# Kernel tuning notes

Hardware: AMD Instinct MI355X
Metric: run time of the kernel (lower is better)

## Reference

```python
import jax, jax.numpy as jnp
import numpy as np
import math

D_MODEL = 1024
N_HEADS = 16
HEAD_DIM = D_MODEL // N_HEADS
FF_DIM = 4096
EPS = 1e-5


def setup_inputs() -> dict:
    key = jax.random.key(0)
    ks = jax.random.split(key, 18)
    s = 0.02
    inp = {
        "x": jax.random.normal(ks[0], (4, 2048, D_MODEL), dtype=jnp.float32),
        "wq": jax.random.normal(ks[1], (D_MODEL, D_MODEL), dtype=jnp.float32) * s,
        "bq": jnp.zeros((D_MODEL,), jnp.float32),
        "wk": jax.random.normal(ks[2], (D_MODEL, D_MODEL), dtype=jnp.float32) * s,
        "bk": jnp.zeros((D_MODEL,), jnp.float32),
        "wv": jax.random.normal(ks[3], (D_MODEL, D_MODEL), dtype=jnp.float32) * s,
        "bv": jnp.zeros((D_MODEL,), jnp.float32),
        "wo": jax.random.normal(ks[4], (D_MODEL, D_MODEL), dtype=jnp.float32) * s,
        "bo": jnp.zeros((D_MODEL,), jnp.float32),
        "w1": jax.random.normal(ks[5], (FF_DIM, D_MODEL), dtype=jnp.float32) * s,
        "b1": jnp.zeros((FF_DIM,), jnp.float32),
        "w2": jax.random.normal(ks[6], (D_MODEL, FF_DIM), dtype=jnp.float32) * s,
        "b2": jnp.zeros((D_MODEL,), jnp.float32),
        "g1": jnp.ones((D_MODEL,), jnp.float32),
        "beta1": jnp.zeros((D_MODEL,), jnp.float32),
        "g2": jnp.ones((D_MODEL,), jnp.float32),
        "beta2": jnp.zeros((D_MODEL,), jnp.float32),
    }
    return inp


def _layernorm(x, g, b):
    mu = jnp.mean(x, axis=-1, keepdims=True)
    var = jnp.mean(jnp.square(x - mu), axis=-1, keepdims=True)
    return (x - mu) * jax.lax.rsqrt(var + EPS) * g + b


def _block(x, wq, bq, wk, bk, wv, bv, wo, bo, w1, b1, w2, b2, g1, beta1, g2, beta2):
    B, S, _ = x.shape
    # projections (torch Linear: x @ W.T + b)
    q = (x @ wq.T + bq).reshape(B, S, N_HEADS, HEAD_DIM)
    k = (x @ wk.T + bk).reshape(B, S, N_HEADS, HEAD_DIM)
    v = (x @ wv.T + bv).reshape(B, S, N_HEADS, HEAD_DIM)
    scores = jnp.einsum("bqhd,bkhd->bhqk", q, k) / math.sqrt(HEAD_DIM)
    attn = jax.nn.softmax(scores, axis=-1)
    o = jnp.einsum("bhqk,bkhd->bqhd", attn, v).reshape(B, S, D_MODEL)
    attn_out = o @ wo.T + bo
    x = _layernorm(x + attn_out, g1, beta1)
    h = jax.nn.gelu(x @ w1.T + b1, approximate=False)
    ff = h @ w2.T + b2
    return _layernorm(x + ff, g2, beta2)


def reference(x, wq, bq, wk, bk, wv, bv, wo, bo, w1, b1, w2, b2, g1, beta1, g2, beta2):
    return _block(x, wq, bq, wk, bk, wv, bv, wo, bo, w1, b1, w2, b2, g1, beta1, g2, beta2)
```

## Files before the change

kernel.cpp:

```cpp
#include <hip/hip_runtime.h>
#include <hip/hip_bf16.h>
#include <math.h>


typedef __attribute__((ext_vector_type(8))) short short8;
typedef __attribute__((ext_vector_type(4))) float f32x4;

__device__ __forceinline__ unsigned short f2bf(float f) {
  unsigned int u = __builtin_bit_cast(unsigned int, f);
  u = (u + 0x7fffu + ((u >> 16) & 1u)) >> 16;
  return (unsigned short)u;
}
__device__ __forceinline__ float bf2f(unsigned short h) {
  unsigned int u = ((unsigned int)h) << 16;
  return __builtin_bit_cast(float, u);
}
__device__ __forceinline__ f32x4 mfma16(short8 a, short8 b, f32x4 c) {
  return __builtin_amdgcn_mfma_f32_16x16x32_bf16(a, b, c, 0, 0, 0);
}
__device__ __forceinline__ void gload16(const void* g, void* l) {
  __builtin_amdgcn_global_load_lds((const __attribute__((address_space(1))) void*)g,
                                   (__attribute__((address_space(3))) void*)l, 16, 0, 0);
}

__global__ void cast_f32_bf16(const float* __restrict__ in,
                              unsigned short* __restrict__ out, int n4) {
  for (int i = blockIdx.x * blockDim.x + threadIdx.x; i < n4;
       i += gridDim.x * blockDim.x) {
    float4 v = ((const float4*)in)[i];
    ushort4 o;
    o.x = f2bf(v.x); o.y = f2bf(v.y); o.z = f2bf(v.z); o.w = f2bf(v.w);
    ((ushort4*)out)[i] = o;
  }
}

template<int EPI>
__global__ void gemm_bt(const unsigned short* __restrict__ A,
                        const unsigned short* __restrict__ W,
                        const float* __restrict__ bias,
                        unsigned short* __restrict__ C,
                        int M, int N, int K) {
  __shared__ unsigned short As[128 * 64];
  __shared__ unsigned short Bs[128 * 64];
  const int t = threadIdx.x;
  const int lane = t & 63, w = t >> 6;
  const int l15 = lane & 15, l4 = lane >> 4;
  const int m0 = blockIdx.y * 128, n0 = blockIdx.x * 128;
  const int wr = (w >> 1) * 64, wc = (w & 1) * 64;
  f32x4 acc[4][4] = {};
  const int srow = t >> 3;
  const int scol = (t & 7) * 16;

  for (int k0 = 0; k0 < K; k0 += 64) {
    __syncthreads();
#pragma unroll
    for (int r = 0; r < 4; ++r) {
      int row = r * 32 + srow;
      gload16((const char*)(A + (size_t)(m0 + row) * K + k0) + scol,
              (char*)As + row * 128 + scol);
    }
#pragma unroll
    for (int r = 0; r < 4; ++r) {
      int row = r * 32 + srow;
      gload16((const char*)(W + (size_t)(n0 + row) * K + k0) + scol,
              (char*)Bs + row * 128 + scol);
    }
    __syncthreads();
#pragma unroll
    for (int ks = 0; ks < 2; ++ks) {
      short8 af[4], bfr[4];
#pragma unroll
      for (int m = 0; m < 4; ++m)
        af[m] = *(const short8*)((const char*)As + (wr + m * 16 + l15) * 128 +
                                 ks * 64 + l4 * 16);
#pragma unroll
      for (int n = 0; n < 4; ++n)
        bfr[n] = *(const short8*)((const char*)Bs + (wc + n * 16 + l15) * 128 +
                                  ks * 64 + l4 * 16);
#pragma unroll
      for (int m = 0; m < 4; ++m)
#pragma unroll
        for (int n = 0; n < 4; ++n)
          acc[m][n] = mfma16(af[m], bfr[n], acc[m][n]);
    }
  }
#pragma unroll
  for (int n = 0; n < 4; ++n) {
    int col = n0 + wc + n * 16 + l15;
    float bcol = bias[col];
#pragma unroll
    for (int m = 0; m < 4; ++m) {
      int row = m0 + wr + m * 16 + l4 * 4;
#pragma unroll
      for (int j = 0; j < 4; ++j) {
        float v = acc[m][n][j] + bcol;
        if (EPI == 1) v = 0.5f * v * (1.0f + erff(v * 0.70710678118654752f));
        if (EPI == 2) v *= 0.125f;
        C[(size_t)(row + j) * N + col] = f2bf(v);
      }
    }
  }
}

__global__ void transpose_v(const unsigned short* __restrict__ v,
                            unsigned short* __restrict__ vt) {
  __shared__ unsigned short tile[64][66];
  const int bh = blockIdx.y;
  const int b = bh >> 4, h = bh & 15;
  const int s0 = blockIdx.x * 64;
  const int t = threadIdx.x;
  const int sr = t >> 2;
  const int dc = (t & 3) * 16;
  const unsigned short* src =
      v + ((size_t)(b * 2048 + s0 + sr) * 1024 + h * 64 + dc);
  short8 a0 = *(const short8*)src;
  short8 a1 = *(const short8*)(src + 8);
#pragma unroll
  for (int i = 0; i < 8; ++i) tile[sr][dc + i] = (unsigned short)a0[i];
#pragma unroll
  for (int i = 0; i < 8; ++i) tile[sr][dc + 8 + i] = (unsigned short)a1[i];
  __syncthreads();
  const int dr = t >> 2;
  const int sc = (t & 3) * 16;
  short8 o0, o1;
#pragma unroll
  for (int i = 0; i < 8; ++i) o0[i] = (short)tile[sc + i][dr];
#pragma unroll
  for (int i = 0; i < 8; ++i) o1[i] = (short)tile[sc + 8 + i][dr];
  unsigned short* dst = vt + ((size_t)(bh * 64 + dr) * 2048 + s0 + sc);
  *(short8*)dst = o0;
  *(short8*)(dst + 8) = o1;
}

__global__ void attn_fwd(const unsigned short* __restrict__ Q,
                         const unsigned short* __restrict__ K,
                         const unsigned short* __restrict__ Vt,
                         unsigned short* __restrict__ O) {
  __shared__ unsigned short Ks[64 * 64];
  __shared__ unsigned short Vs[64 * 64];
  __shared__ unsigned short Ps[4][32 * 64];
  const int bh = blockIdx.y;
  const int b = bh >> 4, h = bh & 15;
  const int q0 = blockIdx.x * 128;
  const int t = threadIdx.x;
  const int lane = t & 63, w = t >> 6;
  const int l15 = lane & 15, l4 = lane >> 4;
  const int swl = (l15 & 7) << 4;

  short8 qf[2][2];
#pragma unroll
  for (int m = 0; m < 2; ++m) {
    const unsigned short* qp =
        Q + ((size_t)(b * 2048 + q0 + w * 32 + m * 16 + l15) * 1024 +
             h * 64 + l4 * 8);
    qf[m][0] = *(const short8*)qp;
    qf[m][1] = *(const short8*)(qp + 32);
  }

  f32x4 o_acc[2][4] = {};
  float l_part[2][4] = {};

  const int srow = t >> 3;
  const int schk = t & 7;
  unsigned short* pw = &Ps[w][0];

#pragma unroll 1
  for (int kt = 0; kt < 32; ++kt) {
    __syncthreads();
#pragma unroll
    for (int r = 0; r < 2; ++r) {
      int row = r * 32 + srow;
      int gofs = (schk ^ (row & 7)) << 4;
      gload16((const char*)(K + (size_t)(b * 2048 + kt * 64 + row) * 1024 +
                            h * 64) + gofs,
              (char*)Ks + row * 128 + schk * 16);
      gload16((const char*)(Vt + (size_t)(bh * 64 + row) * 2048 + kt * 64) + gofs,
              (char*)Vs + row * 128 + schk * 16);
    }
    __syncthreads();

    f32x4 s_acc[2][4] = {};
#pragma unroll
    for (int c = 0; c < 4; ++c) {
      const char* krow = (const char*)Ks + (c * 16 + l15) * 128;
      short8 kf0 = *(const short8*)(krow + ((l4 * 16) ^ swl));
      short8 kf1 = *(const short8*)(krow + ((64 + l4 * 16) ^ swl));
#pragma unroll
      for (int m = 0; m < 2; ++m) {
        s_acc[m][c] = mfma16(qf[m][0], kf0, s_acc[m][c]);
        s_acc[m][c] = mfma16(qf[m][1], kf1, s_acc[m][c]);
      }
    }
#pragma unroll
    for (int m = 0; m < 2; ++m) {
#pragma unroll
      for (int j = 0; j < 4; ++j) {
        float p0 = __expf(s_acc[m][0][j]);
        float p1 = __expf(s_acc[m][1][j]);
        float p2 = __expf(s_acc[m][2][j]);
        float p3 = __expf(s_acc[m][3][j]);
        l_part[m][j] += (p0 + p1) + (p2 + p3);
        int row = m * 16 + l4 * 4 + j;
        int swr = (row & 7) << 4;
        char* pr = (char*)pw + row * 128;
        *(unsigned short*)(pr + ((l15 * 2) ^ swr))      = f2bf(p0);
        *(unsigned short*)(pr + ((32 + l15 * 2) ^ swr)) = f2bf(p1);
        *(unsigned short*)(pr + ((64 + l15 * 2) ^ swr)) = f2bf(p2);
        *(unsigned short*)(pr + ((96 + l15 * 2) ^ swr)) = f2bf(p3);
      }
    }
#pragma unroll
    for (int ks = 0; ks < 2; ++ks) {
      short8 pf[2];
#pragma unroll
      for (int m = 0; m < 2; ++m)
        pf[m] = *(const short8*)((const char*)pw + (m * 16 + l15) * 128 +
                                 ((ks * 64 + l4 * 16) ^ swl));
#pragma unroll
      for (int c = 0; c < 4; ++c) {
        short8 vf = *(const short8*)((const char*)Vs + (c * 16 + l15) * 128 +
                                     ((ks * 64 + l4 * 16) ^ swl));
#pragma unroll
        for (int m = 0; m < 2; ++m)
          o_acc[m][c] = mfma16(pf[m], vf, o_acc[m][c]);
      }
    }
  }
#pragma unroll
  for (int m = 0; m < 2; ++m) {
#pragma unroll
    for (int j = 0; j < 4; ++j) {
      float l = l_part[m][j];
      l += __shfl_xor(l, 1, 64);
      l += __shfl_xor(l, 2, 64);
      l += __shfl_xor(l, 4, 64);
      l += __shfl_xor(l, 8, 64);
      float inv = 1.0f / l;
      int row = b * 2048 + q0 + w * 32 + m * 16 + l4 * 4 + j;
#pragma unroll
      for (int c = 0; c < 4; ++c) {
        int col = h * 64 + c * 16 + l15;
        O[(size_t)row * 1024 + col] = f2bf(o_acc[m][c][j] * inv);
      }
    }
  }
}

__global__ void add_ln(const float* __restrict__ res,
                       const unsigned short* __restrict__ delta,
                       const float* __restrict__ g,
                       const float* __restrict__ beta,
                       float* __restrict__ out_f32,
                       unsigned short* __restrict__ out_bf) {
  __shared__ float red1[4], red2[4];
  const int row = blockIdx.x;
  const int t = threadIdx.x;
  const int lane = t & 63, w = t >> 6;
  const size_t base = (size_t)row * 1024 + t * 4;
  float4 rv = *(const float4*)(res + base);
  ushort4 dv = *(const ushort4*)(delta + base);
  float v0 = rv.x + bf2f(dv.x);
  float v1 = rv.y + bf2f(dv.y);
  float v2 = rv.z + bf2f(dv.z);
  float v3 = rv.w + bf2f(dv.w);
  float s = v0 + v1 + v2 + v3;
#pragma unroll
  for (int m = 1; m <= 32; m <<= 1) s += __shfl_xor(s, m, 64);
  if (lane == 0) red1[w] = s;
  __syncthreads();
  float mean = (red1[0] + red1[1] + red1[2] + red1[3]) * (1.0f / 1024.0f);
  float d0 = v0 - mean, d1 = v1 - mean, d2 = v2 - mean, d3 = v3 - mean;
  float q = d0 * d0 + d1 * d1 + d2 * d2 + d3 * d3;
#pragma unroll
  for (int m = 1; m <= 32; m <<= 1) q += __shfl_xor(q, m, 64);
  if (lane == 0) red2[w] = q;
  __syncthreads();
  float var = (red2[0] + red2[1] + red2[2] + red2[3]) * (1.0f / 1024.0f);
  float rstd = rsqrtf(var + 1e-5f);
  float4 gv = *(const float4*)(g + t * 4);
  float4 bv = *(const float4*)(beta + t * 4);
  float y0 = d0 * rstd * gv.x + bv.x;
  float y1 = d1 * rstd * gv.y + bv.y;
  float y2 = d2 * rstd * gv.z + bv.z;
  float y3 = d3 * rstd * gv.w + bv.w;
  float4 ov = {y0, y1, y2, y3};
  *(float4*)(out_f32 + base) = ov;
  if (out_bf) {
    ushort4 obv;
    obv.x = f2bf(y0); obv.y = f2bf(y1); obv.z = f2bf(y2); obv.w = f2bf(y3);
    *(ushort4*)(out_bf + base) = obv;
  }
}

extern "C" void kernel_launch(void* const* d_in, const int* in_sizes, int n_in,
                              void* d_out, int out_size, void* d_ws, size_t ws_size,
                              hipStream_t stream) {
  const float* x   = (const float*)d_in[0];
  const float* wq  = (const float*)d_in[1];
  const float* bq  = (const float*)d_in[2];
  const float* wk  = (const float*)d_in[3];
  const float* bk  = (const float*)d_in[4];
  const float* wv  = (const float*)d_in[5];
  const float* bv  = (const float*)d_in[6];
  const float* wo  = (const float*)d_in[7];
  const float* bo  = (const float*)d_in[8];
  const float* w1  = (const float*)d_in[9];
  const float* b1  = (const float*)d_in[10];
  const float* w2  = (const float*)d_in[11];
  const float* b2  = (const float*)d_in[12];
  const float* g1  = (const float*)d_in[13];
  const float* be1 = (const float*)d_in[14];
  const float* g2  = (const float*)d_in[15];
  const float* be2 = (const float*)d_in[16];
  float* out = (float*)d_out;

  char* wsb = (char*)d_ws;
  const size_t MB = 1ull << 20;
  unsigned short* x_bf  = (unsigned short*)(wsb + 0 * MB);
  unsigned short* qb    = (unsigned short*)(wsb + 16 * MB);
  unsigned short* kb    = (unsigned short*)(wsb + 32 * MB);
  unsigned short* vb    = (unsigned short*)(wsb + 48 * MB);
  unsigned short* vt    = (unsigned short*)(wsb + 64 * MB);
  unsigned short* ob    = (unsigned short*)(wsb + 80 * MB);
  unsigned short* hb    = (unsigned short*)(wsb + 0 * MB);
  unsigned short* ff_bf = (unsigned short*)(wsb + 64 * MB);
  unsigned short* wq_bf = (unsigned short*)(wsb + 96 * MB);
  unsigned short* wk_bf = (unsigned short*)(wsb + 98 * MB);
  unsigned short* wv_bf = (unsigned short*)(wsb + 100 * MB);
  unsigned short* wo_bf = (unsigned short*)(wsb + 102 * MB);
  unsigned short* w1_bf = (unsigned short*)(wsb + 104 * MB);
  unsigned short* w2_bf = (unsigned short*)(wsb + 112 * MB);
  unsigned short* ao_bf = (unsigned short*)(wsb + 120 * MB);
  float*          x1    = (float*)(wsb + 136 * MB);
  unsigned short* x1_bf = (unsigned short*)(wsb + 168 * MB);

  auto cast = [&](const float* in, unsigned short* o, int n) {
    int n4 = n / 4;
    int blocks = (n4 + 255) / 256;
    if (blocks > 2048) blocks = 2048;
    cast_f32_bf16<<<blocks, 256, 0, stream>>>(in, o, n4);
  };
  cast(x, x_bf, 4 * 2048 * 1024);
  cast(wq, wq_bf, 1024 * 1024);
  cast(wk, wk_bf, 1024 * 1024);
  cast(wv, wv_bf, 1024 * 1024);
  cast(wo, wo_bf, 1024 * 1024);
  cast(w1, w1_bf, 4096 * 1024);
  cast(w2, w2_bf, 1024 * 4096);

  dim3 blk(256);
  gemm_bt<2><<<dim3(8, 64), blk, 0, stream>>>(x_bf, wq_bf, bq, qb, 8192, 1024, 1024);
  gemm_bt<0><<<dim3(8, 64), blk, 0, stream>>>(x_bf, wk_bf, bk, kb, 8192, 1024, 1024);
  gemm_bt<0><<<dim3(8, 64), blk, 0, stream>>>(x_bf, wv_bf, bv, vb, 8192, 1024, 1024);
  transpose_v<<<dim3(32, 64), blk, 0, stream>>>(vb, vt);
  attn_fwd<<<dim3(16, 64), blk, 0, stream>>>(qb, kb, vt, ob);
  gemm_bt<0><<<dim3(8, 64), blk, 0, stream>>>(ob, wo_bf, bo, ao_bf, 8192, 1024, 1024);
  add_ln<<<8192, blk, 0, stream>>>(x, ao_bf, g1, be1, x1, x1_bf);
  gemm_bt<1><<<dim3(32, 64), blk, 0, stream>>>(x1_bf, w1_bf, b1, hb, 8192, 4096, 1024);
  gemm_bt<0><<<dim3(8, 64), blk, 0, stream>>>(hb, w2_bf, b2, ff_bf, 8192, 1024, 4096);
  add_ln<<<8192, blk, 0, stream>>>(x1, ff_bf, g2, be2, out, (unsigned short*)nullptr);
}
```

Baseline: 621.0 us.

## Use 256x256-tile 8-wave pipelined GEMM for FFN up-projection

Adds a new GEMM kernel with 256x256 output tiles, 512 threads (8 waves), double-buffered LDS filled by direct global-to-LDS loads with XOR swizzle, and fine-grained interleaving of staging and MFMA phases using barriers, waitcnt and setprio. It also remaps block IDs across XCDs. It replaces the 128-tile GEMM only for the w1 projection with GELU epilogue, aiming for higher data reuse and overlap of loads with compute. It uses 128KB of LDS and many accumulator registers, and the hand-tuned vmcnt counts are fragile.

Measured after the change: 633.7 us. 2.0% more time.

```diff
diff --git a/kernel.cpp b/kernel.cpp
--- a/kernel.cpp
+++ b/kernel.cpp
@@ -99,6 +99,165 @@
         C[(size_t)(row + j) * N + col] = f2bf(v);
       }
     }
+  }
+}
+
+template<int EPI>
+__global__ __launch_bounds__(512, 2)
+void gemm_bt8(const unsigned short* __restrict__ A,
+              const unsigned short* __restrict__ W,
+              const float* __restrict__ bias,
+              unsigned short* __restrict__ C,
+              int M, int N, int K, int nbx) {
+  __shared__ unsigned short lds[2][2][256 * 64];
+  const int t = threadIdx.x;
+  const int lane = t & 63, wid = t >> 6;
+  const int wm = wid >> 2, wn = wid & 3;
+  const int l15 = lane & 15, l4 = lane >> 4;
+  const int rchk = l15 & 7;
+  const int nwg = gridDim.x, cpx = nwg >> 3;
+  const int orig = blockIdx.x;
+  const int bid = (orig & 7) * cpx + (orig >> 3);
+  const int m0 = (bid / nbx) * 256, n0 = (bid % nbx) * 256;
+  const int NT = K >> 6;
+
+  auto stageA = [&](int buf, int half, int Tt) {
+#pragma unroll
+    for (int i = 0; i < 2; ++i) {
+      int q = t + 512 * i;
+      int rl = q >> 3, c = q & 7;
+      int row = half * 64 + (rl & 63) + (rl >> 6) * 128;
+      int gc = (c ^ (row & 7)) * 16;
+      gload16((const char*)(A + (size_t)(m0 + row) * K + Tt * 64) + gc,
+              (char*)&lds[buf][0][0] + row * 128 + c * 16);
+    }
+  };
+  auto stageB = [&](int buf, int half, int Tt) {
+#pragma unroll
+    for (int i = 0; i < 2; ++i) {
+      int q = t + 512 * i;
+      int rl = q >> 3, c = q & 7;
+      int row = half * 128 + rl;
+      int gc = (c ^ (row & 7)) * 16;
+      gload16((const char*)(W + (size_t)(n0 + row) * K + Tt * 64) + gc,
+              (char*)&lds[buf][1][0] + row * 128 + c * 16);
+    }
+  };
+
+  f32x4 acc[8][4] = {};
+  short8 bfr[2][4];
+
+  stageA(0, 0, 0); stageB(0, 0, 0); stageB(0, 1, 0); stageA(0, 1, 0);
+  if (NT > 1) { stageA(1, 0, 1); stageB(1, 0, 1); }
+  asm volatile("s_waitcnt vmcnt(4)" ::: "memory");
+  __builtin_amdgcn_s_barrier();
+
+  for (int T = 0; T < NT; ++T) {
+    const int buf = T & 1;
+    const char* Ab = (const char*)&lds[buf][0][0];
+    const char* Bb = (const char*)&lds[buf][1][0];
+    const bool sK1 = (T + 1) < NT, sK2 = (T + 2) < NT;
+    const bool tail = (T >= NT - 3);
+    short8 af[4];
+
+    if (sK1) stageB(buf ^ 1, 1, T + 1);
+#pragma unroll
+    for (int n = 0; n < 4; ++n)
+      bfr[0][n] = *(const short8*)(Bb + (wn * 64 + n * 16 + l15) * 128 +
+                                   ((l4 ^ rchk) * 16));
+#pragma unroll
+    for (int m = 0; m < 4; ++m)
+      af[m] = *(const short8*)(Ab + (wm * 128 + m * 16 + l15) * 128 +
+                               ((l4 ^ rchk) * 16));
+    __builtin_amdgcn_s_barrier();
+    asm volatile("s_waitcnt lgkmcnt(0)" ::: "memory");
+    __builtin_amdgcn_sched_barrier(0);
+    __builtin_amdgcn_s_setprio(1);
+#pragma unroll
+    for (int m = 0; m < 4; ++m)
+#pragma unroll
+      for (int n = 0; n < 4; ++n)
+        acc[m][n] = mfma16(af[m], bfr[0][n], acc[m][n]);
+    __builtin_amdgcn_s_setprio(0);
+    __builtin_amdgcn_s_barrier();
+
+    if (sK1) stageA(buf ^ 1, 1, T + 1);
+#pragma unroll
+    for (int n = 0; n < 4; ++n)
+      bfr[1][n] = *(const short8*)(Bb + (wn * 64 + n * 16 + l15) * 128 +
+                                   (((4 + l4) ^ rchk) * 16));
+#pragma unroll
+    for (int m = 0; m < 4; ++m)
+      af[m] = *(const short8*)(Ab + (wm * 128 + m * 16 + l15) * 128 +
+                               (((4 + l4) ^ rchk) * 16));
+    __builtin_amdgcn_s_barrier();
+    asm volatile("s_waitcnt lgkmcnt(0)" ::: "memory");
+    __builtin_amdgcn_sched_barrier(0);
+    __builtin_amdgcn_s_setprio(1);
+#pragma unroll
+    for (int m = 0; m < 4; ++m)
+#pragma unroll
+      for (int n = 0; n < 4; ++n)
+        acc[m][n] = mfma16(af[m], bfr[1][n], acc[m][n]);
+    __builtin_amdgcn_s_setprio(0);
+    if (tail) asm volatile("s_waitcnt vmcnt(0)" ::: "memory");
+    else      asm volatile("s_waitcnt vmcnt(8)" ::: "memory");
+    __builtin_amdgcn_s_barrier();
+
+    if (sK2) stageA(buf, 0, T + 2);
+#pragma unroll
+    for (int m = 0; m < 4; ++m)
+      af[m] = *(const short8*)(Ab + (wm * 128 + 64 + m * 16 + l15) * 128 +
+                               ((l4 ^ rchk) * 16));
+    __builtin_amdgcn_s_barrier();
+    asm volatile("s_waitcnt lgkmcnt(0)" ::: "memory");
+    __builtin_amdgcn_sched_barrier(0);
+    __builtin_amdgcn_s_setprio(1);
+#pragma unroll
+    for (int m = 0; m < 4; ++m)
+#pragma unroll
+      for (int n = 0; n < 4; ++n)
+        acc[4 + m][n] = mfma16(af[m], bfr[0][n], acc[4 + m][n]);
+    __builtin_amdgcn_s_setprio(0);
+    __builtin_amdgcn_s_barrier();
+
+    if (sK2) stageB(buf, 0, T + 2);
+#pragma unroll
+    for (int m = 0; m < 4; ++m)
+      af[m] = *(const short8*)(Ab + (wm * 128 + 64 + m * 16 + l15) * 128 +
+                               (((4 + l4) ^ rchk) * 16));
+    __builtin_amdgcn_s_barrier();
+    asm volatile("s_waitcnt lgkmcnt(0)" ::: "memory");
+    __builtin_amdgcn_sched_barrier(0);
+    __builtin_amdgcn_s_setprio(1);
+#pragma unroll
+    for (int m = 0; m < 4; ++m)
+#pragma unroll
+      for (int n = 0; n < 4; ++n)
+        acc[4 + m][n] = mfma16(af[m], bfr[1][n], acc[4 + m][n]);
+    __builtin_amdgcn_s_setprio(0);
+    if (tail) asm volatile("s_waitcnt vmcnt(0)" ::: "memory");
+    else      asm volatile("s_waitcnt vmcnt(6)" ::: "memory");
+    __builtin_amdgcn_s_barrier();
+  }
+
+#pragma unroll
+  for (int n = 0; n < 4; ++n) {
+    int col = n0 + wn * 64 + n * 16 + l15;
+    float bcol = bias[col];
+#pragma unroll
+    for (int mh = 0; mh < 2; ++mh)
+#pragma unroll
+      for (int m = 0; m < 4; ++m) {
+        int row = m0 + wm * 128 + mh * 64 + m * 16 + l4 * 4;
+#pragma unroll
+        for (int j = 0; j < 4; ++j) {
+          float v = acc[mh * 4 + m][n][j] + bcol;
+          if (EPI == 1) v = 0.5f * v * (1.0f + erff(v * 0.70710678118654752f));
+          if (EPI == 2) v *= 0.125f;
+          C[(size_t)(row + j) * N + col] = f2bf(v);
+        }
+      }
   }
 }
 
@@ -356,7 +515,7 @@
   attn_fwd<<<dim3(16, 64), blk, 0, stream>>>(qb, kb, vt, ob);
   gemm_bt<0><<<dim3(8, 64), blk, 0, stream>>>(ob, wo_bf, bo, ao_bf, 8192, 1024, 1024);
   add_ln<<<8192, blk, 0, stream>>>(x, ao_bf, g1, be1, x1, x1_bf);
-  gemm_bt<1><<<dim3(32, 64), blk, 0, stream>>>(x1_bf, w1_bf, b1, hb, 8192, 4096, 1024);
+  gemm_bt8<1><<<512, 512, 0, stream>>>(x1_bf, w1_bf, b1, hb, 8192, 4096, 1024, 16);
   gemm_bt<0><<<dim3(8, 64), blk, 0, stream>>>(hb, w2_bf, b2, ff_bf, 8192, 1024, 4096);
   add_ln<<<8192, blk, 0, stream>>>(x1, ff_bf, g2, be2, out, (unsigned short*)nullptr);
 }
```

## Prefetch next K/V tile into registers during attention compute; pack bf16 converts

Applied to the files above, without the earlier changes.

Replaces the direct global-to-LDS loads at the top of each key tile with register prefetch. The next tile's K and V are loaded into registers while the current tile is computed, then written to swizzled LDS after a barrier, so global latency overlaps the MFMA and softmax work. The probability conversion also switches to the hardware packed bf16 convert instruction in place of manual rounding. The trade is higher register pressure, which may lower occupancy, and the extra LDS write pass through VGPRs.

After: 792.0 us. 27.5% more time.

```diff
diff --git a/kernel.cpp b/kernel.cpp
--- a/kernel.cpp
+++ b/kernel.cpp
@@ -164,20 +164,34 @@
   const int schk = t & 7;
   unsigned short* pw = &Ps[w][0];
 
+  uint4 kreg[2], vreg[2];
+  auto issue = [&](int kt) {
+#pragma unroll
+    for (int r = 0; r < 2; ++r) {
+      int row = r * 32 + srow;
+      kreg[r] = *(const uint4*)((const char*)(K + (size_t)(b * 2048 + kt * 64 +
+                                row) * 1024 + h * 64) + schk * 16);
+      vreg[r] = *(const uint4*)((const char*)(Vt + (size_t)(bh * 64 + row) *
+                                2048 + kt * 64) + schk * 16);
+    }
+  };
+  auto commit = [&]() {
+#pragma unroll
+    for (int r = 0; r < 2; ++r) {
+      int row = r * 32 + srow;
+      int c = (schk ^ (row & 7)) * 16;
+      *(uint4*)((char*)Ks + row * 128 + c) = kreg[r];
+      *(uint4*)((char*)Vs + row * 128 + c) = vreg[r];
+    }
+  };
+
+  issue(0);
+  commit();
+  __syncthreads();
+
 #pragma unroll 1
   for (int kt = 0; kt < 32; ++kt) {
-    __syncthreads();
-#pragma unroll
-    for (int r = 0; r < 2; ++r) {
-      int row = r * 32 + srow;
-      int gofs = (schk ^ (row & 7)) << 4;
-      gload16((const char*)(K + (size_t)(b * 2048 + kt * 64 + row) * 1024 +
-                            h * 64) + gofs,
-              (char*)Ks + row * 128 + schk * 16);
-      gload16((const char*)(Vt + (size_t)(bh * 64 + row) * 2048 + kt * 64) + gofs,
-              (char*)Vs + row * 128 + schk * 16);
-    }
-    __syncthreads();
+    if (kt + 1 < 32) issue(kt + 1);
 
     f32x4 s_acc[2][4] = {};
 #pragma unroll
@@ -200,13 +214,16 @@
         float p2 = __expf(s_acc[m][2][j]);
         float p3 = __expf(s_acc[m][3][j]);
         l_part[m][j] += (p0 + p1) + (p2 + p3);
+        unsigned int pk01, pk23;
+        asm("v_cvt_pk_bf16_f32 %0, %1, %2" : "=v"(pk01) : "v"(p0), "v"(p1));
+        asm("v_cvt_pk_bf16_f32 %0, %1, %2" : "=v"(pk23) : "v"(p2), "v"(p3));
         int row = m * 16 + l4 * 4 + j;
         int swr = (row & 7) << 4;
         char* pr = (char*)pw + row * 128;
-        *(unsigned short*)(pr + ((l15 * 2) ^ swr))      = f2bf(p0);
-        *(unsigned short*)(pr + ((32 + l15 * 2) ^ swr)) = f2bf(p1);
-        *(unsigned short*)(pr + ((64 + l15 * 2) ^ swr)) = f2bf(p2);
-        *(unsigned short*)(pr + ((96 + l15 * 2) ^ swr)) = f2bf(p3);
+        *(unsigned short*)(pr + ((l15 * 2) ^ swr))      = (unsigned short)pk01;
+        *(unsigned short*)(pr + ((32 + l15 * 2) ^ swr)) = (unsigned short)(pk01 >> 16);
+        *(unsigned short*)(pr + ((64 + l15 * 2) ^ swr)) = (unsigned short)pk23;
+        *(unsigned short*)(pr + ((96 + l15 * 2) ^ swr)) = (unsigned short)(pk23 >> 16);
       }
     }
 #pragma unroll
@@ -225,6 +242,9 @@
           o_acc[m][c] = mfma16(pf[m], vf, o_acc[m][c]);
       }
     }
+    __syncthreads();
+    if (kt + 1 < 32) commit();
+    __syncthreads();
   }
 #pragma unroll
   for (int m = 0; m < 2; ++m) {
```
